# Kernel optimization log

Measured on AMD Instinct MI355X. Metric: run time of the kernel, lower is better.

## Reference

```python
import jax, jax.numpy as jnp
import numpy as np

N_FEATURES = 784   # binary tabular features (MNIST-like)
Z_DIM = 64         # latent dim fed to decoder net
BX = 256           # number of data points x
BZ = 4096          # number of latent samples / components z


def setup_inputs() -> dict:
    key = jax.random.key(0)
    k1, k2, k3 = jax.random.split(key, 3)
    x = jax.random.uniform(k1, (BX, N_FEATURES), dtype=jnp.float32)  # soft targets in [0,1)
    z = jax.random.normal(k2, (BZ, Z_DIM), dtype=jnp.float32)
    # net := Linear(Z_DIM -> 2*N_FEATURES)
    W = jax.random.normal(k3, (Z_DIM, 2 * N_FEATURES), dtype=jnp.float32) * 0.05
    b = jnp.zeros((2 * N_FEATURES,), dtype=jnp.float32)
    # chain-structured CLT: root = feature 0 (parent -1), feature i's parent is i-1
    tree = jnp.concatenate([jnp.array([-1], dtype=jnp.int32),
                            jnp.arange(N_FEATURES - 1, dtype=jnp.int32)])
    return {"x": x, "z": z, "W": W, "b": b, "tree": tree}


def reference(x, z, W, b, tree):
    F = tree.shape[0]
    # net(z) -> logits_p [Bz, F, 2]
    logits_p = (z @ W + b).reshape(-1, F, 2)
    # _preprocess_logits_p: at root, copy state-1 logit into state-0 slot
    root_mask = (tree == -1)  # [F]
    lp0 = jnp.where(root_mask[None, :], logits_p[:, :, 1], logits_p[:, :, 0])
    logits_p = jnp.stack([lp0, logits_p[:, :, 1]], axis=-1)  # [Bz, F, 2]
    # parent-conditioned selector x_cond [Bx, F, 2]
    xt = x[:, tree]  # gather parent values; -1 at root wraps (same as torch)
    x_cond = jnp.stack([1.0 - xt, xt], axis=-1)
    # bce (negative binary cross-entropy = Bernoulli log-likelihood):
    #   lls[b,i,j,k] = x[b,j]*log_sigmoid(lp[i,j,k]) + (1-x[b,j])*log_sigmoid(-lp[i,j,k])
    # (x_doubled duplicates x along k, so both k slots use x[b,j])
    # Then einsum('bijk,bjk->bij', lls, x_cond).sum(-1). Distribute x_cond to
    # avoid materializing the [Bx,Bz,F,2] lls tensor (same math, fused):
    ls = jax.nn.log_sigmoid(logits_p)     # [Bz, F, 2]
    lsn = jax.nn.log_sigmoid(-logits_p)   # [Bz, F, 2]
    a = x_cond * x[:, :, None]            # [Bx, F, 2]
    c = x_cond * (1.0 - x)[:, :, None]    # [Bx, F, 2]
    log_prob_bins = (jnp.einsum('bjk,ijk->bi', a, ls)
                     + jnp.einsum('bjk,ijk->bi', c, lsn))  # [Bx, Bz]
    return log_prob_bins
```

## Files before the change

### kernel.cpp

```cpp
#include <hip/hip_runtime.h>

#define NF   784
#define ZD   64
#define BXN  256
#define BZN  4096
#define KDIM 3136
#define LCOL 1568

typedef __attribute__((ext_vector_type(8))) short bf16x8;
typedef __attribute__((ext_vector_type(4))) float f32x4;
typedef __attribute__((ext_vector_type(8))) unsigned short ushort8;

__device__ __forceinline__ unsigned short f2bf(float f) {
  unsigned u = __float_as_uint(f);
  u += 0x7fff + ((u >> 16) & 1);
  return (unsigned short)(u >> 16);
}

__global__ __launch_bounds__(256) void prep(const float* __restrict__ x,
                                            const float* __restrict__ z,
                                            const float* __restrict__ W,
                                            const int* __restrict__ tree,
                                            unsigned short* __restrict__ Amat,
                                            unsigned short* __restrict__ zb,
                                            unsigned short* __restrict__ Wt) {
  int bid = blockIdx.x, tid = threadIdx.x;
  if (bid < 1024) {
    int b = bid >> 2;
    int j = (bid & 3) * 256 + tid;
    if (j >= NF) return;
    float xb = x[b * NF + j];
    int idx = tree[j];
    int gidx = idx < 0 ? idx + NF : idx;
    float xt = x[b * NF + gidx];
    ushort4 v;
    v.x = f2bf((1.f - xt) * xb);
    v.y = f2bf(xt * xb);
    v.z = f2bf((1.f - xt) * (1.f - xb));
    v.w = f2bf(xt * (1.f - xb));
    *(ushort4*)&Amat[(size_t)b * KDIM + 4 * j] = v;
  } else if (bid < 1280) {
    int t = (bid - 1024) * 256 + tid;
    float4 v = *(const float4*)&z[t * 4];
    ushort4 o = { f2bf(v.x), f2bf(v.y), f2bf(v.z), f2bf(v.w) };
    *(ushort4*)&zb[t * 4] = o;
  } else {
    int t = (bid - 1280) * 256 + tid;
    int c = t >> 4, k0 = (t & 15) * 4;
    ushort4 o;
    o.x = f2bf(W[(k0 + 0) * LCOL + c]);
    o.y = f2bf(W[(k0 + 1) * LCOL + c]);
    o.z = f2bf(W[(k0 + 2) * LCOL + c]);
    o.w = f2bf(W[(k0 + 3) * LCOL + c]);
    *(ushort4*)&Wt[c * 64 + k0] = o;
  }
}

#define LP 40
__global__ __launch_bounds__(256) void gemm_fused(const unsigned short* __restrict__ Amat,
                                                  const unsigned short* __restrict__ zb,
                                                  const unsigned short* __restrict__ Wt,
                                                  const float* __restrict__ bias,
                                                  const int* __restrict__ tree,
                                                  float* __restrict__ part) {
  __shared__ unsigned short As[256][LP];
  __shared__ unsigned short Bs[64][LP];
  int bid = blockIdx.x;
  int s = bid & 7, nt = bid >> 3;
  int n0 = nt * 64;
  int kt0 = s * 12 + (s < 2 ? s : 2);
  int nsteps = (s < 2) ? 13 : 12;
  int tid = threadIdx.x;
  int w = tid >> 6, lane = tid & 63;
  int fr = lane & 15, hi = lane >> 4, kq = hi * 8;
  int srow = tid >> 2, scol = (tid & 3) * 8;
  const unsigned short* Ag = Amat + (size_t)srow * KDIM + scol;

  const unsigned short* zp = zb + (size_t)(n0 + w * 16 + fr) * 64 + kq;
  bf16x8 zf0 = *(const bf16x8*)zp;
  bf16x8 zf1 = *(const bf16x8*)(zp + 32);

  f32x4 acc[4][4];
#pragma unroll
  for (int m = 0; m < 4; ++m)
#pragma unroll
    for (int n = 0; n < 4; ++n) acc[m][n] = (f32x4){0.f, 0.f, 0.f, 0.f};

  for (int kt = kt0; kt < kt0 + nsteps; ++kt) {
    int k0 = kt * 32;
    float4 ar[4];
#pragma unroll
    for (int q = 0; q < 4; ++q)
      ar[q] = *(const float4*)(Ag + (size_t)q * 64 * KDIM + k0);
    const unsigned short* wp = Wt + (size_t)(kt * 16 + fr) * 64 + kq;
    bf16x8 wf0 = *(const bf16x8*)wp;
    bf16x8 wf1 = *(const bf16x8*)(wp + 32);
    f32x4 lacc = (f32x4){0.f, 0.f, 0.f, 0.f};
    lacc = __builtin_amdgcn_mfma_f32_16x16x32_bf16(wf0, zf0, lacc, 0, 0, 0);
    lacc = __builtin_amdgcn_mfma_f32_16x16x32_bf16(wf1, zf1, lacc, 0, 0, 0);
    float4 b4 = *(const float4*)&bias[kt * 16 + 4 * hi];
    int2 tr2 = *(const int2*)&tree[kt * 8 + 2 * hi];
    float bb[4] = { b4.x, b4.y, b4.z, b4.w };
    int tt[2] = { tr2.x, tr2.y };
    ushort8 v;
#pragma unroll
    for (int p = 0; p < 2; ++p) {
      float l1 = lacc[2 * p + 1] + bb[2 * p + 1];
      float l0 = (tt[p] == -1) ? l1 : (lacc[2 * p] + bb[2 * p]);
      float e0 = __expf(-fabsf(l0)); float sp0 = __logf(1.f + e0);
      float ls0 = (l0 >= 0.f) ? -sp0 : l0 - sp0;
      float e1 = __expf(-fabsf(l1)); float sp1 = __logf(1.f + e1);
      float ls1 = (l1 >= 0.f) ? -sp1 : l1 - sp1;
      v[4 * p + 0] = f2bf(ls0);
      v[4 * p + 1] = f2bf(ls1);
      v[4 * p + 2] = f2bf(ls0 - l0);
      v[4 * p + 3] = f2bf(ls1 - l1);
    }
#pragma unroll
    for (int q = 0; q < 4; ++q)
      *(float4*)&As[srow + q * 64][scol] = ar[q];
    *(ushort8*)&Bs[w * 16 + fr][kq] = v;
    __syncthreads();
    bf16x8 a[4], b[4];
#pragma unroll
    for (int m = 0; m < 4; ++m) a[m] = *(const bf16x8*)&As[w * 64 + m * 16 + fr][kq];
#pragma unroll
    for (int n = 0; n < 4; ++n) b[n] = *(const bf16x8*)&Bs[n * 16 + fr][kq];
#pragma unroll
    for (int m = 0; m < 4; ++m)
#pragma unroll
      for (int n = 0; n < 4; ++n)
        acc[m][n] = __builtin_amdgcn_mfma_f32_16x16x32_bf16(a[m], b[n], acc[m][n], 0, 0, 0);
    __syncthreads();
  }
  int col = lane & 15, rq = hi * 4;
  float* Pp = part + (size_t)s * (256 * 4096) + (size_t)(w * 64) * 4096 + n0;
#pragma unroll
  for (int m = 0; m < 4; ++m)
#pragma unroll
    for (int n = 0; n < 4; ++n)
#pragma unroll
      for (int r = 0; r < 4; ++r)
        Pp[(m * 16 + rq + r) * 4096 + n * 16 + col] = acc[m][n][r];
}

__global__ __launch_bounds__(256) void reduce8(const float* __restrict__ part,
                                               float* __restrict__ out) {
  int t = blockIdx.x * 256 + threadIdx.x;
  f32x4 s = (f32x4){0.f, 0.f, 0.f, 0.f};
#pragma unroll
  for (int q = 0; q < 8; ++q)
    s += *(const f32x4*)&part[(size_t)q * (256 * 4096) + (size_t)t * 4];
  *(f32x4*)&out[(size_t)t * 4] = s;
}

extern "C" void kernel_launch(void* const* d_in, const int* in_sizes, int n_in,
                              void* d_out, int out_size, void* d_ws, size_t ws_size,
                              hipStream_t stream) {
  const float* x    = (const float*)d_in[0];
  const float* z    = (const float*)d_in[1];
  const float* W    = (const float*)d_in[2];
  const float* bias = (const float*)d_in[3];
  const int*   tree = (const int*)d_in[4];
  float* out = (float*)d_out;

  unsigned short* Amat = (unsigned short*)d_ws;
  unsigned short* zb   = (unsigned short*)((char*)d_ws + 1605632);
  unsigned short* Wt   = (unsigned short*)((char*)d_ws + 2129920);
  float*          part = (float*)((char*)d_ws + 2330624);

  prep<<<dim3(1378), 256, 0, stream>>>(x, z, W, tree, Amat, zb, Wt);
  gemm_fused<<<dim3(512), 256, 0, stream>>>(Amat, zb, Wt, bias, tree, part);
  reduce8<<<dim3(1024), 256, 0, stream>>>(part, out);
}
```

Baseline: 44.74 us.

## Double-buffer LDS tiles and prefetch next K-step operands in fused GEMM

Doubles the LDS tiles for A and the computed log-sigmoid B tile so one barrier per K-step is enough, dropping the trailing __syncthreads. The global loads of the A tile, W fragments, bias and tree values for the next step are issued before the current step's transcendental work and MFMAs, so their latency overlaps with compute. In exchange it uses twice the LDS and more registers for the prefetched values, which may lower occupancy.

```diff
diff --git a/kernel.cpp b/kernel.cpp
--- a/kernel.cpp
+++ b/kernel.cpp
@@ -63,13 +63,14 @@
                                                   const float* __restrict__ bias,
                                                   const int* __restrict__ tree,
                                                   float* __restrict__ part) {
-  __shared__ unsigned short As[256][LP];
-  __shared__ unsigned short Bs[64][LP];
+  __shared__ unsigned short As[2][256][LP];
+  __shared__ unsigned short Bs[2][64][LP];
   int bid = blockIdx.x;
   int s = bid & 7, nt = bid >> 3;
   int n0 = nt * 64;
   int kt0 = s * 12 + (s < 2 ? s : 2);
   int nsteps = (s < 2) ? 13 : 12;
+  int ktend = kt0 + nsteps;
   int tid = threadIdx.x;
   int w = tid >> 6, lane = tid & 63;
   int fr = lane & 15, hi = lane >> 4, kq = hi * 8;
@@ -86,20 +87,34 @@
 #pragma unroll
     for (int n = 0; n < 4; ++n) acc[m][n] = (f32x4){0.f, 0.f, 0.f, 0.f};
 
-  for (int kt = kt0; kt < kt0 + nsteps; ++kt) {
-    int k0 = kt * 32;
-    float4 ar[4];
-#pragma unroll
-    for (int q = 0; q < 4; ++q)
-      ar[q] = *(const float4*)(Ag + (size_t)q * 64 * KDIM + k0);
-    const unsigned short* wp = Wt + (size_t)(kt * 16 + fr) * 64 + kq;
-    bf16x8 wf0 = *(const bf16x8*)wp;
-    bf16x8 wf1 = *(const bf16x8*)(wp + 32);
+  const unsigned short* wp = Wt + (size_t)(kt0 * 16 + fr) * 64 + kq;
+  bf16x8 wf0 = *(const bf16x8*)wp;
+  bf16x8 wf1 = *(const bf16x8*)(wp + 32);
+  float4 b4  = *(const float4*)&bias[kt0 * 16 + 4 * hi];
+  int2   tr2 = *(const int2*)&tree[kt0 * 8 + 2 * hi];
+  int k0 = kt0 * 32;
+  float4 ar0 = *(const float4*)(Ag + k0);
+  float4 ar1 = *(const float4*)(Ag + (size_t)64 * KDIM + k0);
+  float4 ar2 = *(const float4*)(Ag + (size_t)128 * KDIM + k0);
+  float4 ar3 = *(const float4*)(Ag + (size_t)192 * KDIM + k0);
+
+  int buf = 0;
+  for (int i = 0; i < nsteps; ++i) {
+    int kt = kt0 + i;
     f32x4 lacc = (f32x4){0.f, 0.f, 0.f, 0.f};
     lacc = __builtin_amdgcn_mfma_f32_16x16x32_bf16(wf0, zf0, lacc, 0, 0, 0);
     lacc = __builtin_amdgcn_mfma_f32_16x16x32_bf16(wf1, zf1, lacc, 0, 0, 0);
-    float4 b4 = *(const float4*)&bias[kt * 16 + 4 * hi];
-    int2 tr2 = *(const int2*)&tree[kt * 8 + 2 * hi];
+    int ktn = (kt + 1 < ktend) ? kt + 1 : kt;
+    const unsigned short* wpn = Wt + (size_t)(ktn * 16 + fr) * 64 + kq;
+    bf16x8 wfn0 = *(const bf16x8*)wpn;
+    bf16x8 wfn1 = *(const bf16x8*)(wpn + 32);
+    float4 b4n  = *(const float4*)&bias[ktn * 16 + 4 * hi];
+    int2   tr2n = *(const int2*)&tree[ktn * 8 + 2 * hi];
+    int k0n = ktn * 32;
+    float4 arn0 = *(const float4*)(Ag + k0n);
+    float4 arn1 = *(const float4*)(Ag + (size_t)64 * KDIM + k0n);
+    float4 arn2 = *(const float4*)(Ag + (size_t)128 * KDIM + k0n);
+    float4 arn3 = *(const float4*)(Ag + (size_t)192 * KDIM + k0n);
     float bb[4] = { b4.x, b4.y, b4.z, b4.w };
     int tt[2] = { tr2.x, tr2.y };
     ushort8 v;
@@ -116,22 +131,25 @@
       v[4 * p + 2] = f2bf(ls0 - l0);
       v[4 * p + 3] = f2bf(ls1 - l1);
     }
-#pragma unroll
-    for (int q = 0; q < 4; ++q)
-      *(float4*)&As[srow + q * 64][scol] = ar[q];
-    *(ushort8*)&Bs[w * 16 + fr][kq] = v;
+    *(float4*)&As[buf][srow      ][scol] = ar0;
+    *(float4*)&As[buf][srow +  64][scol] = ar1;
+    *(float4*)&As[buf][srow + 128][scol] = ar2;
+    *(float4*)&As[buf][srow + 192][scol] = ar3;
+    *(ushort8*)&Bs[buf][w * 16 + fr][kq] = v;
     __syncthreads();
     bf16x8 a[4], b[4];
 #pragma unroll
-    for (int m = 0; m < 4; ++m) a[m] = *(const bf16x8*)&As[w * 64 + m * 16 + fr][kq];
+    for (int m = 0; m < 4; ++m) a[m] = *(const bf16x8*)&As[buf][w * 64 + m * 16 + fr][kq];
 #pragma unroll
-    for (int n = 0; n < 4; ++n) b[n] = *(const bf16x8*)&Bs[n * 16 + fr][kq];
+    for (int n = 0; n < 4; ++n) b[n] = *(const bf16x8*)&Bs[buf][n * 16 + fr][kq];
 #pragma unroll
     for (int m = 0; m < 4; ++m)
 #pragma unroll
       for (int n = 0; n < 4; ++n)
         acc[m][n] = __builtin_amdgcn_mfma_f32_16x16x32_bf16(a[m], b[n], acc[m][n], 0, 0, 0);
-    __syncthreads();
+    wf0 = wfn0; wf1 = wfn1; b4 = b4n; tr2 = tr2n;
+    ar0 = arn0; ar1 = arn1; ar2 = arn2; ar3 = arn3;
+    buf ^= 1;
   }
   int col = lane & 15, rq = hi * 4;
   float* Pp = part + (size_t)s * (256 * 4096) + (size_t)(w * 64) * 4096 + n0;
```

Result: no change. 44.20 us (-1.2%).

## Load A fragments directly from global, double-buffer B in LDS, use 512-thread blocks

Applied to the files above, without the earlier changes.

The fused GEMM now runs 8 waves per block instead of 4. Each wave owns 32 rows of the A matrix and loads its MFMA fragments straight from global memory, so the A shared-memory tile and its staging copy are gone. Only the first four waves compute the log-sigmoid B tile, which goes into a double-buffered LDS array, and that lets the loop drop from two barriers per step to one. In exchange each wave does more uncoalesced global reads of A, and half the waves sit idle during the B computation.

```diff
diff --git a/kernel.cpp b/kernel.cpp
--- a/kernel.cpp
+++ b/kernel.cpp
@@ -57,14 +57,13 @@
 }
 
 #define LP 40
-__global__ __launch_bounds__(256) void gemm_fused(const unsigned short* __restrict__ Amat,
-                                                  const unsigned short* __restrict__ zb,
-                                                  const unsigned short* __restrict__ Wt,
-                                                  const float* __restrict__ bias,
-                                                  const int* __restrict__ tree,
-                                                  float* __restrict__ part) {
-  __shared__ unsigned short As[256][LP];
-  __shared__ unsigned short Bs[64][LP];
+__global__ __launch_bounds__(512, 4) void gemm_fused(const unsigned short* __restrict__ Amat,
+                                                     const unsigned short* __restrict__ zb,
+                                                     const unsigned short* __restrict__ Wt,
+                                                     const float* __restrict__ bias,
+                                                     const int* __restrict__ tree,
+                                                     float* __restrict__ part) {
+  __shared__ unsigned short Bs[2][64][LP];
   int bid = blockIdx.x;
   int s = bid & 7, nt = bid >> 3;
   int n0 = nt * 64;
@@ -73,75 +72,75 @@
   int tid = threadIdx.x;
   int w = tid >> 6, lane = tid & 63;
   int fr = lane & 15, hi = lane >> 4, kq = hi * 8;
-  int srow = tid >> 2, scol = (tid & 3) * 8;
-  const unsigned short* Ag = Amat + (size_t)srow * KDIM + scol;
 
-  const unsigned short* zp = zb + (size_t)(n0 + w * 16 + fr) * 64 + kq;
-  bf16x8 zf0 = *(const bf16x8*)zp;
-  bf16x8 zf1 = *(const bf16x8*)(zp + 32);
+  bf16x8 zf0, zf1;
+  if (w < 4) {
+    const unsigned short* zp = zb + (size_t)(n0 + w * 16 + fr) * 64 + kq;
+    zf0 = *(const bf16x8*)zp;
+    zf1 = *(const bf16x8*)(zp + 32);
+  }
 
-  f32x4 acc[4][4];
+  const unsigned short* Ag = Amat + (size_t)(w * 32 + fr) * KDIM + kq;
+
+  f32x4 acc[2][4];
 #pragma unroll
-  for (int m = 0; m < 4; ++m)
+  for (int m = 0; m < 2; ++m)
 #pragma unroll
     for (int n = 0; n < 4; ++n) acc[m][n] = (f32x4){0.f, 0.f, 0.f, 0.f};
 
-  for (int kt = kt0; kt < kt0 + nsteps; ++kt) {
+  int buf = 0;
+  for (int i = 0; i < nsteps; ++i) {
+    int kt = kt0 + i;
     int k0 = kt * 32;
-    float4 ar[4];
+    if (w < 4) {
+      const unsigned short* wp = Wt + (size_t)(kt * 16 + fr) * 64 + kq;
+      bf16x8 wf0 = *(const bf16x8*)wp;
+      bf16x8 wf1 = *(const bf16x8*)(wp + 32);
+      f32x4 lacc = (f32x4){0.f, 0.f, 0.f, 0.f};
+      lacc = __builtin_amdgcn_mfma_f32_16x16x32_bf16(wf0, zf0, lacc, 0, 0, 0);
+      lacc = __builtin_amdgcn_mfma_f32_16x16x32_bf16(wf1, zf1, lacc, 0, 0, 0);
+      float4 b4 = *(const float4*)&bias[kt * 16 + 4 * hi];
+      int2 tr2 = *(const int2*)&tree[kt * 8 + 2 * hi];
+      float bb[4] = { b4.x, b4.y, b4.z, b4.w };
+      int tt[2] = { tr2.x, tr2.y };
+      ushort8 v;
 #pragma unroll
-    for (int q = 0; q < 4; ++q)
-      ar[q] = *(const float4*)(Ag + (size_t)q * 64 * KDIM + k0);
-    const unsigned short* wp = Wt + (size_t)(kt * 16 + fr) * 64 + kq;
-    bf16x8 wf0 = *(const bf16x8*)wp;
-    bf16x8 wf1 = *(const bf16x8*)(wp + 32);
-    f32x4 lacc = (f32x4){0.f, 0.f, 0.f, 0.f};
-    lacc = __builtin_amdgcn_mfma_f32_16x16x32_bf16(wf0, zf0, lacc, 0, 0, 0);
-    lacc = __builtin_amdgcn_mfma_f32_16x16x32_bf16(wf1, zf1, lacc, 0, 0, 0);
-    float4 b4 = *(const float4*)&bias[kt * 16 + 4 * hi];
-    int2 tr2 = *(const int2*)&tree[kt * 8 + 2 * hi];
-    float bb[4] = { b4.x, b4.y, b4.z, b4.w };
-    int tt[2] = { tr2.x, tr2.y };
-    ushort8 v;
+      for (int p = 0; p < 2; ++p) {
+        float l1 = lacc[2 * p + 1] + bb[2 * p + 1];
+        float l0 = (tt[p] == -1) ? l1 : (lacc[2 * p] + bb[2 * p]);
+        float e0 = __expf(-fabsf(l0)); float sp0 = __logf(1.f + e0);
+        float ls0 = (l0 >= 0.f) ? -sp0 : l0 - sp0;
+        float e1 = __expf(-fabsf(l1)); float sp1 = __logf(1.f + e1);
+        float ls1 = (l1 >= 0.f) ? -sp1 : l1 - sp1;
+        v[4 * p + 0] = f2bf(ls0);
+        v[4 * p + 1] = f2bf(ls1);
+        v[4 * p + 2] = f2bf(ls0 - l0);
+        v[4 * p + 3] = f2bf(ls1 - l1);
+      }
+      *(ushort8*)&Bs[buf][w * 16 + fr][kq] = v;
+    }
+    bf16x8 a0 = *(const bf16x8*)(Ag + k0);
+    bf16x8 a1 = *(const bf16x8*)(Ag + (size_t)16 * KDIM + k0);
+    __syncthreads();
+    bf16x8 b[4];
 #pragma unroll
-    for (int p = 0; p < 2; ++p) {
-      float l1 = lacc[2 * p + 1] + bb[2 * p + 1];
-      float l0 = (tt[p] == -1) ? l1 : (lacc[2 * p] + bb[2 * p]);
-      float e0 = __expf(-fabsf(l0)); float sp0 = __logf(1.f + e0);
-      float ls0 = (l0 >= 0.f) ? -sp0 : l0 - sp0;
-      float e1 = __expf(-fabsf(l1)); float sp1 = __logf(1.f + e1);
-      float ls1 = (l1 >= 0.f) ? -sp1 : l1 - sp1;
-      v[4 * p + 0] = f2bf(ls0);
-      v[4 * p + 1] = f2bf(ls1);
-      v[4 * p + 2] = f2bf(ls0 - l0);
-      v[4 * p + 3] = f2bf(ls1 - l1);
+    for (int n = 0; n < 4; ++n) b[n] = *(const bf16x8*)&Bs[buf][n * 16 + fr][kq];
+#pragma unroll
+    for (int n = 0; n < 4; ++n) {
+      acc[0][n] = __builtin_amdgcn_mfma_f32_16x16x32_bf16(a0, b[n], acc[0][n], 0, 0, 0);
+      acc[1][n] = __builtin_amdgcn_mfma_f32_16x16x32_bf16(a1, b[n], acc[1][n], 0, 0, 0);
     }
+    buf ^= 1;
+  }
+  float* Pp = part + (size_t)s * (256 * 4096) + (size_t)(w * 32) * 4096 + n0;
+  int rq = hi * 4;
 #pragma unroll
-    for (int q = 0; q < 4; ++q)
-      *(float4*)&As[srow + q * 64][scol] = ar[q];
-    *(ushort8*)&Bs[w * 16 + fr][kq] = v;
-    __syncthreads();
-    bf16x8 a[4], b[4];
-#pragma unroll
-    for (int m = 0; m < 4; ++m) a[m] = *(const bf16x8*)&As[w * 64 + m * 16 + fr][kq];
-#pragma unroll
-    for (int n = 0; n < 4; ++n) b[n] = *(const bf16x8*)&Bs[n * 16 + fr][kq];
-#pragma unroll
-    for (int m = 0; m < 4; ++m)
-#pragma unroll
-      for (int n = 0; n < 4; ++n)
-        acc[m][n] = __builtin_amdgcn_mfma_f32_16x16x32_bf16(a[m], b[n], acc[m][n], 0, 0, 0);
-    __syncthreads();
-  }
-  int col = lane & 15, rq = hi * 4;
-  float* Pp = part + (size_t)s * (256 * 4096) + (size_t)(w * 64) * 4096 + n0;
-#pragma unroll
-  for (int m = 0; m < 4; ++m)
+  for (int m = 0; m < 2; ++m)
 #pragma unroll
     for (int n = 0; n < 4; ++n)
 #pragma unroll
       for (int r = 0; r < 4; ++r)
-        Pp[(m * 16 + rq + r) * 4096 + n * 16 + col] = acc[m][n][r];
+        Pp[(m * 16 + rq + r) * 4096 + n * 16 + fr] = acc[m][n][r];
 }
 
 __global__ __launch_bounds__(256) void reduce8(const float* __restrict__ part,
@@ -170,6 +169,6 @@
   float*          part = (float*)((char*)d_ws + 2330624);
 
   prep<<<dim3(1378), 256, 0, stream>>>(x, z, W, tree, Amat, zb, Wt);
-  gemm_fused<<<dim3(512), 256, 0, stream>>>(Amat, zb, Wt, bias, tree, part);
+  gemm_fused<<<dim3(512), 512, 0, stream>>>(Amat, zb, Wt, bias, tree, part);
   reduce8<<<dim3(1024), 256, 0, stream>>>(part, out);
 }
```

Measured after the change: 47.19 us. +5.5%, slower.
